# Kernel optimization log

Measured on AMD Instinct MI355X. Metric: run time of the kernel, lower is better.

Reference implementation:

```python
import jax, jax.numpy as jnp
import numpy as np

TEMP = 0.07
IGNORE = 255
NUM_CLS = 150   # ADE Challenge classes
VOCAB = 512     # size of the dense idx_star -> cls_idx LUT
B, D, H, W = 4, 512, 256, 256


def setup_inputs() -> dict:
    key = jax.random.key(0)
    k1, k2, k3 = jax.random.split(key, 3)
    pred_embs = jax.random.normal(k1, (B, D, H, W), dtype=jnp.float32)
    # class text embeddings, L2-normalized per class (as in load_ade_challenge_info)
    cls = jax.random.normal(k2, (NUM_CLS, D), dtype=jnp.float32)
    cls_embs = cls / jnp.linalg.norm(cls, axis=1, keepdims=True)
    # idx_star semantic label map, shape (B, 1, H, W)
    idx_star_map = jax.random.randint(k3, (B, 1, H, W), 0, VOCAB, dtype=jnp.int32)
    # dense LUT replacing the python dict idx_star2cls_idx:
    # first NUM_CLS idx_star values map to class indices, the rest are ignored (255)
    ar = jnp.arange(VOCAB, dtype=jnp.int32)
    lut = jnp.where(ar < NUM_CLS, ar, IGNORE).astype(jnp.int32)
    return {"pred_embs": pred_embs, "cls_embs": cls_embs,
            "idx_star_map": idx_star_map, "lut": lut}


def reference(pred_embs, cls_embs, idx_star_map, lut):
    # --- label remap: single gather replaces the per-unique-value mask loop ---
    labels = lut[idx_star_map[:, 0]]                       # (B, H, W) int32
    # --- 1x1 conv == per-pixel dot product with class embeddings ---
    sim = jnp.einsum('bdhw,kd->bkhw', pred_embs, cls_embs) / TEMP  # (B, K, H, W)
    # --- cross-entropy with ignore_index=255 (mean over valid pixels) ---
    logp = jax.nn.log_softmax(sim, axis=1)                 # (B, K, H, W)
    valid = labels != IGNORE
    safe = jnp.where(valid, labels, 0)
    nll = -jnp.take_along_axis(logp, safe[:, None], axis=1)[:, 0]  # (B, H, W)
    n_valid = jnp.sum(valid).astype(nll.dtype)
    return jnp.sum(jnp.where(valid, nll, 0.0)) / n_valid
```

## Files before the change

### kernel.cpp

```cpp
#include <hip/hip_runtime.h>
#include <hip/hip_bf16.h>


#define NUM_CLS 150
#define NT_TILES 5
#define D_DIM   512
#define HW_DIM  65536
#define IGNORE_L 255

typedef __attribute__((ext_vector_type(8)))  short bf16x8;
typedef __attribute__((ext_vector_type(16))) float f32x16;
typedef __attribute__((ext_vector_type(4)))  unsigned int u32x4;

#define GLOAD16(gsrc, ldst) \
    __builtin_amdgcn_global_load_lds((const __attribute__((address_space(1))) void*)(gsrc), \
                                     (__attribute__((address_space(3))) void*)(ldst), 16, 0, 0)

static __device__ __forceinline__ short f2bf(float f) {
    __hip_bfloat16 h = __float2bfloat16(f);
    return __builtin_bit_cast(short, h);
}

__global__ void rsl_pack_cls(const float* __restrict__ cls,
                             unsigned short* __restrict__ packed,
                             double* __restrict__ ws_sum,
                             unsigned long long* __restrict__ ws_cnt)
{
    int t = blockIdx.x * 256 + threadIdx.x;
    if (t == 0) { ws_sum[0] = 0.0; ws_cnt[0] = 0ull; }
    if (t >= 32 * NT_TILES * 64) return;
    int s2 = t / (NT_TILES * 64);
    int r  = t - s2 * (NT_TILES * 64);
    int nt = r >> 6;
    int l  = r & 63;
    int c  = nt * 32 + (l & 31);
    int k  = s2 * 16 + (l >> 5) * 8;
    unsigned short v[8];
#pragma unroll
    for (int j = 0; j < 8; ++j)
        v[j] = (c < NUM_CLS) ? (unsigned short)f2bf(cls[c * D_DIM + k + j]) : (unsigned short)0;
    u32x4 w;
#pragma unroll
    for (int q = 0; q < 4; ++q)
        w[q] = (unsigned int)v[2 * q] | ((unsigned int)v[2 * q + 1] << 16);
    *(u32x4*)(packed + (size_t)(s2 * NT_TILES + nt) * 512 + (size_t)l * 8) = w;
}

__global__ __launch_bounds__(256, 3)
void rsl_mfma(const float* __restrict__ pred,
              const unsigned short* __restrict__ packed,
              const int*   __restrict__ idx,
              const int*   __restrict__ lut,
              double* __restrict__ ws_sum,
              unsigned long long* __restrict__ ws_cnt)
{
    __shared__ float          sP[2][32][128];
    __shared__ unsigned short sC[2][10][512];

    const int lane = threadIdx.x & 63;
    const int wid  = threadIdx.x >> 6;
    const int col  = lane & 31;
    const int hi   = lane >> 5;

    const int pixbase = blockIdx.x * 128;
    const int b  = pixbase >> 16;
    const int p0 = pixbase & 0xFFFF;
    const float* pstage = pred + (size_t)b * D_DIM * HW_DIM
                        + (size_t)(lane >> 5) * HW_DIM + (p0 + (lane & 31) * 4);

    f32x16 acc[NT_TILES] = {};

#pragma unroll
    for (int tt = 0; tt < 4; ++tt) {
        const int t = wid * 4 + tt;
        GLOAD16(pstage + (size_t)(2 * t) * HW_DIM, &sP[0][2 * t][0]);
    }
    for (int i = wid; i < 10; i += 4)
        GLOAD16(packed + (size_t)i * 512 + (size_t)lane * 8, &sC[0][i][0]);
    __syncthreads();

    for (int s = 0; s < 16; ++s) {
        const int cur = s & 1;
        if (s < 15) {
            const float* srcb = pstage + (size_t)((s + 1) * 32) * HW_DIM;
#pragma unroll
            for (int tt = 0; tt < 4; ++tt) {
                const int t = wid * 4 + tt;
                GLOAD16(srcb + (size_t)(2 * t) * HW_DIM, &sP[cur ^ 1][2 * t][0]);
            }
            const unsigned short* csrc = packed + (size_t)((s + 1) * 10) * 512 + (size_t)lane * 8;
            for (int i = wid; i < 10; i += 4)
                GLOAD16(csrc + (size_t)i * 512, &sC[cur ^ 1][i][0]);
        }

#pragma unroll
        for (int ks = 0; ks < 2; ++ks) {
            bf16x8 pf;
#pragma unroll
            for (int j = 0; j < 8; ++j)
                pf[j] = f2bf(sP[cur][ks * 16 + hi * 8 + j][wid * 32 + col]);
#pragma unroll
            for (int nt = 0; nt < NT_TILES; ++nt) {
                bf16x8 cf = *(const bf16x8*)&sC[cur][ks * NT_TILES + nt][lane * 8];
                acc[nt] = __builtin_amdgcn_mfma_f32_32x32x16_bf16(pf, cf, acc[nt], 0, 0, 0);
            }
        }
        __syncthreads();
    }

    const float invT = 1.0f / 0.07f;
    float local_sum = 0.f;
    int   local_cnt = 0;
#pragma unroll
    for (int r = 0; r < 16; ++r) {
        const int prow = (r & 3) + 8 * (r >> 2) + 4 * hi;
        const int pixg = pixbase + wid * 32 + prow;
        const int lab  = lut[idx[pixg]];
        const bool valid = (lab != IGNORE_L);

        float m = -1e30f;
#pragma unroll
        for (int nt = 0; nt < NT_TILES; ++nt) {
            int c = nt * 32 + col;
            float v = (c < NUM_CLS) ? acc[nt][r] : -1e30f;
            m = fmaxf(m, v);
        }
#pragma unroll
        for (int o = 16; o >= 1; o >>= 1) m = fmaxf(m, __shfl_xor(m, o));

        float ssum = 0.f, slab = 0.f;
#pragma unroll
        for (int nt = 0; nt < NT_TILES; ++nt) {
            int c = nt * 32 + col;
            if (c < NUM_CLS) {
                float v = acc[nt][r];
                ssum += __expf((v - m) * invT);
                slab += (c == lab) ? v : 0.f;
            }
        }
#pragma unroll
        for (int o = 16; o >= 1; o >>= 1) {
            ssum += __shfl_xor(ssum, o);
            slab += __shfl_xor(slab, o);
        }
        if (col == 0 && valid) {
            local_sum += (m - slab) * invT + __logf(ssum);
            local_cnt += 1;
        }
    }

#pragma unroll
    for (int o = 32; o >= 1; o >>= 1) {
        local_sum += __shfl_down(local_sum, o);
        local_cnt += __shfl_down(local_cnt, o);
    }
    __shared__ float sv[4];
    __shared__ int   sc[4];
    if (lane == 0) { sv[wid] = local_sum; sc[wid] = local_cnt; }
    __syncthreads();
    if (threadIdx.x == 0) {
        float tv = sv[0] + sv[1] + sv[2] + sv[3];
        int   tc = sc[0] + sc[1] + sc[2] + sc[3];
        atomicAdd(ws_sum, (double)tv);
        atomicAdd(ws_cnt, (unsigned long long)tc);
    }
}

__global__ void rsl_final(const double* __restrict__ ws_sum,
                          const unsigned long long* __restrict__ ws_cnt,
                          float* __restrict__ out)
{
    if (threadIdx.x == 0) {
        double c = (double)ws_cnt[0];
        out[0] = (float)(ws_sum[0] / (c > 0.0 ? c : 1.0));
    }
}

extern "C" void kernel_launch(void* const* d_in, const int* in_sizes, int n_in,
                              void* d_out, int out_size, void* d_ws, size_t ws_size,
                              hipStream_t stream)
{
    const float* pred = (const float*)d_in[0];
    const float* cls  = (const float*)d_in[1];
    const int*   idx  = (const int*)d_in[2];
    const int*   lut  = (const int*)d_in[3];
    float* out = (float*)d_out;

    double* wsd = (double*)d_ws;
    unsigned long long* wsc = (unsigned long long*)((char*)d_ws + 8);
    unsigned short* packed = (unsigned short*)((char*)d_ws + 1024);

    rsl_pack_cls<<<40, 256, 0, stream>>>(cls, packed, wsd, wsc);

    const int total = 4 * HW_DIM;
    rsl_mfma<<<total / 128, 256, 0, stream>>>(pred, packed, idx, lut, wsd, wsc);
    rsl_final<<<1, 64, 0, stream>>>(wsd, wsc, out);
}
```

Baseline: 139.5 us.

## Double pixel tile per block to reuse class fragments across two M-tiles

Each block now covers 256 pixels instead of 128, and each wave computes two 32-pixel M-tiles sharing the same class-embedding fragment. The K loop is split into 32 stages of 16 channels instead of 16 stages of 32, with the LDS layout reshaped to match. This halves class-fragment staging per pixel and grid size. The cost is more accumulator registers (occupancy bound lowered to 2) and twice as many barriers per block.

```diff
diff --git a/kernel.cpp b/kernel.cpp
--- a/kernel.cpp
+++ b/kernel.cpp
@@ -46,7 +46,7 @@
     *(u32x4*)(packed + (size_t)(s2 * NT_TILES + nt) * 512 + (size_t)l * 8) = w;
 }
 
-__global__ __launch_bounds__(256, 3)
+__global__ __launch_bounds__(256, 2)
 void rsl_mfma(const float* __restrict__ pred,
               const unsigned short* __restrict__ packed,
               const int*   __restrict__ idx,
@@ -54,56 +54,58 @@
               double* __restrict__ ws_sum,
               unsigned long long* __restrict__ ws_cnt)
 {
-    __shared__ float          sP[2][32][128];
-    __shared__ unsigned short sC[2][10][512];
+    __shared__ float          sP[2][16][256];
+    __shared__ unsigned short sC[2][NT_TILES][512];
 
     const int lane = threadIdx.x & 63;
     const int wid  = threadIdx.x >> 6;
     const int col  = lane & 31;
     const int hi   = lane >> 5;
 
-    const int pixbase = blockIdx.x * 128;
+    const int pixbase = blockIdx.x * 256;
     const int b  = pixbase >> 16;
     const int p0 = pixbase & 0xFFFF;
-    const float* pstage = pred + (size_t)b * D_DIM * HW_DIM
-                        + (size_t)(lane >> 5) * HW_DIM + (p0 + (lane & 31) * 4);
-
-    f32x16 acc[NT_TILES] = {};
-
-#pragma unroll
-    for (int tt = 0; tt < 4; ++tt) {
-        const int t = wid * 4 + tt;
-        GLOAD16(pstage + (size_t)(2 * t) * HW_DIM, &sP[0][2 * t][0]);
-    }
-    for (int i = wid; i < 10; i += 4)
-        GLOAD16(packed + (size_t)i * 512 + (size_t)lane * 8, &sC[0][i][0]);
+    const float* predb = pred + (size_t)b * D_DIM * HW_DIM + p0;
+
+    f32x16 acc[2][NT_TILES] = {};
+
+#define STAGEP(ss, q) do { \
+    _Pragma("unroll") \
+    for (int tt = 0; tt < 4; ++tt) { \
+        const int d_ = wid * 4 + tt; \
+        GLOAD16(predb + (size_t)((ss) * 16 + d_) * HW_DIM + lane * 4, &sP[q][d_][0]); \
+    } } while (0)
+
+#define STAGEC(ss, q) do { \
+    for (int nt = wid; nt < NT_TILES; nt += 4) \
+        GLOAD16(packed + (size_t)((ss) * NT_TILES + nt) * 512 + (size_t)lane * 8, \
+                &sC[q][nt][0]); \
+    } while (0)
+
+    STAGEP(0, 0);
+    STAGEC(0, 0);
     __syncthreads();
 
-    for (int s = 0; s < 16; ++s) {
+    for (int s = 0; s < 32; ++s) {
         const int cur = s & 1;
-        if (s < 15) {
-            const float* srcb = pstage + (size_t)((s + 1) * 32) * HW_DIM;
-#pragma unroll
-            for (int tt = 0; tt < 4; ++tt) {
-                const int t = wid * 4 + tt;
-                GLOAD16(srcb + (size_t)(2 * t) * HW_DIM, &sP[cur ^ 1][2 * t][0]);
-            }
-            const unsigned short* csrc = packed + (size_t)((s + 1) * 10) * 512 + (size_t)lane * 8;
-            for (int i = wid; i < 10; i += 4)
-                GLOAD16(csrc + (size_t)i * 512, &sC[cur ^ 1][i][0]);
+        if (s < 31) {
+            STAGEP(s + 1, cur ^ 1);
+            STAGEC(s + 1, cur ^ 1);
         }
 
-#pragma unroll
-        for (int ks = 0; ks < 2; ++ks) {
-            bf16x8 pf;
+        bf16x8 pf[2];
+#pragma unroll
+        for (int mt = 0; mt < 2; ++mt)
 #pragma unroll
             for (int j = 0; j < 8; ++j)
-                pf[j] = f2bf(sP[cur][ks * 16 + hi * 8 + j][wid * 32 + col]);
-#pragma unroll
-            for (int nt = 0; nt < NT_TILES; ++nt) {
-                bf16x8 cf = *(const bf16x8*)&sC[cur][ks * NT_TILES + nt][lane * 8];
-                acc[nt] = __builtin_amdgcn_mfma_f32_32x32x16_bf16(pf, cf, acc[nt], 0, 0, 0);
-            }
+                pf[mt][j] = f2bf(sP[cur][hi * 8 + j][wid * 64 + mt * 32 + col]);
+
+#pragma unroll
+        for (int nt = 0; nt < NT_TILES; ++nt) {
+            bf16x8 cf = *(const bf16x8*)&sC[cur][nt][lane * 8];
+#pragma unroll
+            for (int mt = 0; mt < 2; ++mt)
+                acc[mt][nt] = __builtin_amdgcn_mfma_f32_32x32x16_bf16(pf[mt], cf, acc[mt][nt], 0, 0, 0);
         }
         __syncthreads();
     }
@@ -112,40 +114,43 @@
     float local_sum = 0.f;
     int   local_cnt = 0;
 #pragma unroll
-    for (int r = 0; r < 16; ++r) {
-        const int prow = (r & 3) + 8 * (r >> 2) + 4 * hi;
-        const int pixg = pixbase + wid * 32 + prow;
-        const int lab  = lut[idx[pixg]];
-        const bool valid = (lab != IGNORE_L);
-
-        float m = -1e30f;
-#pragma unroll
-        for (int nt = 0; nt < NT_TILES; ++nt) {
-            int c = nt * 32 + col;
-            float v = (c < NUM_CLS) ? acc[nt][r] : -1e30f;
-            m = fmaxf(m, v);
-        }
-#pragma unroll
-        for (int o = 16; o >= 1; o >>= 1) m = fmaxf(m, __shfl_xor(m, o));
-
-        float ssum = 0.f, slab = 0.f;
-#pragma unroll
-        for (int nt = 0; nt < NT_TILES; ++nt) {
-            int c = nt * 32 + col;
-            if (c < NUM_CLS) {
-                float v = acc[nt][r];
-                ssum += __expf((v - m) * invT);
-                slab += (c == lab) ? v : 0.f;
-            }
-        }
-#pragma unroll
-        for (int o = 16; o >= 1; o >>= 1) {
-            ssum += __shfl_xor(ssum, o);
-            slab += __shfl_xor(slab, o);
-        }
-        if (col == 0 && valid) {
-            local_sum += (m - slab) * invT + __logf(ssum);
-            local_cnt += 1;
+    for (int mt = 0; mt < 2; ++mt) {
+#pragma unroll
+        for (int r = 0; r < 16; ++r) {
+            const int prow = (r & 3) + 8 * (r >> 2) + 4 * hi;
+            const int pixg = pixbase + wid * 64 + mt * 32 + prow;
+            const int lab  = lut[idx[pixg]];
+            const bool valid = (lab != IGNORE_L);
+
+            float m = -1e30f;
+#pragma unroll
+            for (int nt = 0; nt < NT_TILES; ++nt) {
+                int c = nt * 32 + col;
+                float v = (c < NUM_CLS) ? acc[mt][nt][r] : -1e30f;
+                m = fmaxf(m, v);
+            }
+#pragma unroll
+            for (int o = 16; o >= 1; o >>= 1) m = fmaxf(m, __shfl_xor(m, o));
+
+            float ssum = 0.f, slab = 0.f;
+#pragma unroll
+            for (int nt = 0; nt < NT_TILES; ++nt) {
+                int c = nt * 32 + col;
+                if (c < NUM_CLS) {
+                    float v = acc[mt][nt][r];
+                    ssum += __expf((v - m) * invT);
+                    slab += (c == lab) ? v : 0.f;
+                }
+            }
+#pragma unroll
+            for (int o = 16; o >= 1; o >>= 1) {
+                ssum += __shfl_xor(ssum, o);
+                slab += __shfl_xor(slab, o);
+            }
+            if (col == 0 && valid) {
+                local_sum += (m - slab) * invT + __logf(ssum);
+                local_cnt += 1;
+            }
         }
     }
 
@@ -193,6 +198,6 @@
     rsl_pack_cls<<<40, 256, 0, stream>>>(cls, packed, wsd, wsc);
 
     const int total = 4 * HW_DIM;
-    rsl_mfma<<<total / 128, 256, 0, stream>>>(pred, packed, idx, lut, wsd, wsc);
+    rsl_mfma<<<total / 256, 256, 0, stream>>>(pred, packed, idx, lut, wsd, wsc);
     rsl_final<<<1, 64, 0, stream>>>(wsd, wsc, out);
 }
```

New measurement: 137.2 us. Within noise of the previous version (-1.7%).
